# Kernel optimization log

Measured on AMD Instinct MI355X. Metric: run time of the kernel, lower is better.

Reference implementation:

```python
import jax, jax.numpy as jnp
import numpy as np

MAX_SPAN_WIDTH = 12
THRESHOLD = 0.5


def _span_table(num_words):
    starts, ends = [], []
    for s in range(num_words):
        for e in range(s, min(num_words, s + MAX_SPAN_WIDTH)):
            starts.append(s)
            ends.append(e)
    return np.asarray(starts, np.int32), np.asarray(ends, np.int32)


def _mlp(x, w1, b1, w2, b2):
    # Linear -> LeakyReLU(0.01) -> Linear
    return jax.nn.leaky_relu(x @ w1 + b1, negative_slope=0.01) @ w2 + b2


def setup_inputs() -> dict:
    B, L, H, E, W, DFF = 8, 1024, 768, 16, 504, 512
    key = jax.random.key(0)
    ks = jax.random.split(key, 9)
    hidden_states = jax.random.normal(ks[0], (B, L, H), dtype=jnp.float32)
    # layout: first E tokens are entity-type tokens, next 2*W tokens are text (2 subwords/word)
    ent_mask = np.zeros((B, L), np.int32); ent_mask[:, :E] = 1
    text_mask = np.zeros((B, L), np.int32); text_mask[:, E:E + 2 * W] = 1
    word_index = np.full((B, L), -1, np.int32)
    word_index[:, E:E + 2 * W] = np.repeat(np.arange(W, dtype=np.int32), 2)[None, :]
    s = 0.02
    return {
        "hidden_states": hidden_states,
        "ent_w1": jax.random.normal(ks[1], (H, DFF), jnp.float32) * s,
        "ent_b1": jnp.zeros((DFF,), jnp.float32),
        "ent_w2": jax.random.normal(ks[2], (DFF, H), jnp.float32) * s,
        "ent_b2": jnp.zeros((H,), jnp.float32),
        "span_w1": jax.random.normal(ks[3], (2 * H, DFF), jnp.float32) * s,
        "span_b1": jnp.zeros((DFF,), jnp.float32),
        "span_w2": jax.random.normal(ks[4], (DFF, H), jnp.float32) * s,
        "span_b2": jnp.zeros((H,), jnp.float32),
        "text_mask": jnp.asarray(text_mask),
        "ent_mask": jnp.asarray(ent_mask),
        "word_index": jnp.asarray(word_index),
        "num_words": W,
        "num_ent": E,
    }


def reference(hidden_states, ent_w1, ent_b1, ent_w2, ent_b2,
              span_w1, span_b1, span_w2, span_b2,
              text_mask, ent_mask, word_index, num_words, num_ent):
    B, L, H = hidden_states.shape
    W, E = int(num_words), int(num_ent)

    # ---- word-level mean pooling over subword tokens (WordTokenRepresentation) ----
    valid = (text_mask == 1) & (word_index >= 0)                       # [B,L]
    oh = ((word_index[..., None] == jnp.arange(W)) & valid[..., None]).astype(hidden_states.dtype)  # [B,L,W]
    counts = jnp.maximum(oh.sum(axis=1), 1.0)                          # [B,W]
    word_emb = jnp.einsum('blw,blh->bwh', oh, hidden_states) / counts[..., None]

    # ---- gather entity-type tokens in order (EntityTokenRepresentation) ----
    keyv = jnp.where(ent_mask == 1, jnp.arange(L), L + jnp.arange(L))
    ent_pos = jnp.argsort(keyv, axis=-1)[:, :E]                        # [B,E]
    ent_tok = jnp.take_along_axis(hidden_states, ent_pos[..., None], axis=1)  # [B,E,H]
    ent_vec = _mlp(ent_tok, ent_w1, ent_b1, ent_w2, ent_b2)            # [B,E,H]

    # ---- span representations (all spans of width < MAX_SPAN_WIDTH) ----
    starts_np, ends_np = _span_table(W)                                # [N]
    span_in = jnp.concatenate([word_emb[:, starts_np], word_emb[:, ends_np]], axis=-1)  # [B,N,2H]
    span_vec = _mlp(span_in, span_w1, span_b1, span_w2, span_b2)       # [B,N,H]

    # ---- matching logits ----
    logits = jnp.einsum('bnh,beh->bne', span_vec, ent_vec)             # [B,N,E]

    # ---- NMS-style greedy decode (flat mode): threshold + score sort + overlap rejection ----
    N = logits.shape[1]
    probs = jax.nn.sigmoid(logits).reshape(B, N * E)
    cstart = jnp.repeat(jnp.asarray(starts_np), E)                     # [N*E]
    cend = jnp.repeat(jnp.asarray(ends_np), E)
    order = jnp.argsort(-probs, axis=-1)                               # score-descending
    probs_s = jnp.take_along_axis(probs, order, axis=-1)
    s_s, e_s = cstart[order], cend[order]
    pos = jnp.arange(W)

    def decode_one(pr, ss, ee):
        def body(cov, x):
            p, s, e = x
            m = (pos >= s) & (pos <= e)                                # candidate span mask over words
            take = (p > THRESHOLD) & ~jnp.any(cov & m)                 # flat: reject any overlap
            return cov | (m & take), take
        _, taken = jax.lax.scan(body, jnp.zeros((W,), bool), (pr, ss, ee))
        return taken

    taken_sorted = jax.vmap(decode_one)(probs_s, s_s, e_s)             # [B,N*E]
    inv = jnp.argsort(order, axis=-1)
    selected = jnp.take_along_axis(taken_sorted, inv, axis=-1).reshape(B, N, E)
    return logits, selected
```

## Files before the change

### kernel.cpp

```cpp
#include <hip/hip_runtime.h>
#include <hip/hip_bf16.h>
#include <stdint.h>

#define B_ 8
#define L_ 1024
#define H_ 768
#define E_ 16
#define W_ 504
#define DFF_ 512
#define N_ 5982
#define NE_ (N_*E_)
#define BNE_ (B_*NE_)
#define MAXC_ 6144
#define MAXK48 0x0000FFFFFFFFFFFFull
#define PT_ 24

typedef unsigned long long u64;
typedef unsigned int u32;

__device__ __forceinline__ int rowstart_of(int s){
    int s0 = W_ - 11;
    if (s <= s0) return 12*s;
    int t = s - s0;
    return 12*s0 + t*11 - (t*(t-1))/2;
}

__device__ __forceinline__ u64 shflup_u64(u64 x, int d){
    u32 lo = (u32)__shfl_up((int)(u32)x, d, 64);
    u32 hi = (u32)__shfl_up((int)(u32)(x >> 32), d, 64);
    return ((u64)hi << 32) | (u64)lo;
}
__device__ __forceinline__ u64 shflxor_u64(u64 x, int m){
    u32 lo = (u32)__shfl_xor((int)(u32)x, m, 64);
    u32 hi = (u32)__shfl_xor((int)(u32)(x >> 32), m, 64);
    return ((u64)hi << 32) | (u64)lo;
}

__global__ void k_prolog(const int* __restrict__ ent_mask, int* __restrict__ ent_pos,
                         int* __restrict__ starts, int* __restrict__ ends,
                         int* __restrict__ tokc){
    int blk = blockIdx.x; int tid = threadIdx.x;
    if (blk == 8){
        for (int s = tid; s < W_; s += 256){
            int rs = rowstart_of(s);
            int cnt = min(12, W_ - s);
            for (int i = 0; i < cnt; i++){ starts[rs+i] = s; ends[rs+i] = s+i; }
        }
        for (int i = tid; i < B_*W_; i += 256) tokc[i] = 0;
        return;
    }
    __shared__ u32 wt[4]; __shared__ u32 cbase;
    int b = blk;
    int lane = tid & 63, wave = tid >> 6;
    if (tid == 0) cbase = 0;
    __syncthreads();
    for (int base = 0; base < L_; base += 256){
        int l = base + tid;
        bool f = (ent_mask[b*L_ + l] == 1);
        u64 bal = __ballot(f);
        if (lane == 0) wt[wave] = (u32)__popcll(bal);
        __syncthreads();
        u32 pre = cbase;
        for (int w = 0; w < 4; w++) if (w < wave) pre += wt[w];
        if (f){
            u32 rank = pre + (u32)__popcll(bal & ((1ull<<lane)-1ull));
            if (rank < E_) ent_pos[b*E_ + rank] = l;
        }
        __syncthreads();
        if (tid == 0){ u32 r = cbase; for (int w = 0; w < 4; w++) r += wt[w]; cbase = r; }
        __syncthreads();
    }
    u32 totEnt = cbase;
    if (totEnt >= E_) return;
    for (int base = 0; base < L_; base += 256){
        int l = base + tid;
        bool f = (ent_mask[b*L_ + l] != 1);
        u64 bal = __ballot(f);
        if (lane == 0) wt[wave] = (u32)__popcll(bal);
        __syncthreads();
        u32 pre = cbase;
        for (int w = 0; w < 4; w++) if (w < wave) pre += wt[w];
        if (f){
            u32 rank = pre + (u32)__popcll(bal & ((1ull<<lane)-1ull));
            if (rank < E_) ent_pos[b*E_ + rank] = l;
        }
        __syncthreads();
        if (tid == 0){ u32 r = cbase; for (int w = 0; w < 4; w++) r += wt[w]; cbase = r; }
        __syncthreads();
    }
}

__global__ void k_toklist(const int* __restrict__ tm, const int* __restrict__ wi,
                          int* __restrict__ tok, int* __restrict__ tokc){
    int i = blockIdx.x*256 + threadIdx.x;
    if (i >= B_*L_) return;
    int w = wi[i];
    if (tm[i] == 1 && w >= 0 && w < W_){
        int b = i / L_;
        int bw = b*W_ + w;
        int pos = atomicAdd(&tokc[bw], 1);
        if (pos < 4) tok[bw*4 + pos] = i - b*L_;
    }
}

__global__ void k_poolsort(const float* __restrict__ hs, const int* __restrict__ tok,
                           const int* __restrict__ tokc, float* __restrict__ wemb){
    __shared__ int stok[4]; __shared__ int scnt;
    int bw = blockIdx.x;
    int b = bw / W_;
    int tid = threadIdx.x;
    if (tid == 0){
        int c = tokc[bw]; int cc = min(c, 4);
        int v[4];
        for (int k = 0; k < cc; k++) v[k] = tok[bw*4 + k];
        for (int a = 1; a < cc; a++){ int x = v[a]; int j = a-1; while (j >= 0 && v[j] > x){ v[j+1] = v[j]; j--; } v[j+1] = x; }
        for (int k = 0; k < cc; k++) stok[k] = v[k];
        scnt = c;
    }
    __syncthreads();
    int c = scnt; int cc = min(c, 4);
    float denom = (float)max(c, 1);
    for (int h = tid; h < H_; h += 256){
        double s = 0.0;
        for (int k = 0; k < cc; k++)
            s += (double)hs[((size_t)(b*L_ + stok[k]))*H_ + h];
        wemb[(size_t)bw*H_ + h] = (float)(s / (double)denom);
    }
}

__global__ void k_ent1(const float* __restrict__ hs, const int* __restrict__ ent_pos,
                       const float* __restrict__ w1, const float* __restrict__ b1,
                       float* __restrict__ hidg){
    __shared__ float x[H_];
    int blk = blockIdx.x;
    int be = blk >> 1; int half = blk & 1;
    int b = be >> 4;
    int tid = threadIdx.x;
    int pos = ent_pos[be];
    const float* xp = hs + ((size_t)b*L_ + pos)*H_;
    for (int j = tid; j < H_; j += 256) x[j] = xp[j];
    __syncthreads();
    int d = half*256 + tid;
    float a0=0.f,a1=0.f,a2=0.f,a3=0.f;
    const float* wp = w1 + d;
    #pragma unroll 8
    for (int h = 0; h < H_; h += 4){
        a0 += x[h+0]*wp[(size_t)(h+0)*DFF_];
        a1 += x[h+1]*wp[(size_t)(h+1)*DFF_];
        a2 += x[h+2]*wp[(size_t)(h+2)*DFF_];
        a3 += x[h+3]*wp[(size_t)(h+3)*DFF_];
    }
    float acc = ((a0+a1)+(a2+a3)) + b1[d];
    hidg[(size_t)be*DFF_ + d] = acc > 0.f ? acc : 0.01f*acc;
}

__global__ void k_ent2(const float* __restrict__ hidg,
                       const float* __restrict__ w2, const float* __restrict__ b2,
                       float* __restrict__ ent_vec){
    __shared__ float hsd[DFF_];
    int blk = blockIdx.x;
    int be = blk / 3; int third = blk % 3;
    int tid = threadIdx.x;
    const float* hp = hidg + (size_t)be*DFF_;
    for (int j = tid; j < DFF_; j += 256) hsd[j] = hp[j];
    __syncthreads();
    int j = third*256 + tid;
    float a0=0.f,a1=0.f,a2=0.f,a3=0.f;
    const float* wp = w2 + j;
    #pragma unroll 8
    for (int d = 0; d < DFF_; d += 4){
        a0 += hsd[d+0]*wp[(size_t)(d+0)*H_];
        a1 += hsd[d+1]*wp[(size_t)(d+1)*H_];
        a2 += hsd[d+2]*wp[(size_t)(d+2)*H_];
        a3 += hsd[d+3]*wp[(size_t)(d+3)*H_];
    }
    ent_vec[(size_t)be*H_ + j] = ((a0+a1)+(a2+a3)) + b2[j];
}

__global__ void k_Mc(const float* __restrict__ span_w2, const float* __restrict__ span_b2,
                     const float* __restrict__ ent_vec, float* __restrict__ M,
                     float* __restrict__ cvec){
    int blk = blockIdx.x;
    if (blk == 256){
        int i = threadIdx.x;
        if (i < B_*E_){
            const float* ev = ent_vec + (size_t)i*H_;
            double acc = 0.0;
            for (int h = 0; h < H_; h++) acc += (double)span_b2[h]*(double)ev[h];
            cvec[i] = (float)acc;
        }
        return;
    }
    int b = blk/32; int dbase = (blk%32)*16;
    int tid = threadIdx.x; int d = dbase + (tid>>4); int e = tid&15;
    const float* ev = ent_vec + ((size_t)b*E_ + e)*H_;
    const float* wr = span_w2 + (size_t)d*H_;
    double p0=0.0, p1=0.0;
    for (int h = 0; h < H_; h += 2){
        p0 += (double)wr[h]*(double)ev[h];
        p1 += (double)wr[h+1]*(double)ev[h+1];
    }
    M[((size_t)b*DFF_ + d)*E_ + e] = (float)(p0+p1);
}

__global__ void k_pq(const float* __restrict__ wemb, const float* __restrict__ w1,
                     float* __restrict__ PQ, int b0){
    __shared__ float As[16][68];
    __shared__ float Bs[16][68];
    int bx = blockIdx.x & 15;
    int by = blockIdx.x >> 4;
    int tid = threadIdx.x;
    int tm = tid >> 4, tn = tid & 15;
    const float* A0 = wemb + (size_t)b0*W_*H_;
    int colbase = bx*64;
    const float* Bbase = (colbase < DFF_) ? w1 : (w1 + (size_t)H_*DFF_);
    int bcol0 = (colbase < DFF_) ? colbase : (colbase - DFF_);
    float acc[4][4] = {{0.f}};
    int ar = tid >> 2, akq = tid & 3;
    int bkk = tid >> 4, bcq = tid & 15;
    const int ROWS = 4*W_;
    for (int k0 = 0; k0 < H_; k0 += 16){
        {
            int gr = by*64 + ar;
            float4 av;
            if (gr < ROWS) av = *(const float4*)(A0 + (size_t)gr*H_ + k0 + akq*4);
            else av = make_float4(0.f,0.f,0.f,0.f);
            As[akq*4+0][ar] = av.x; As[akq*4+1][ar] = av.y;
            As[akq*4+2][ar] = av.z; As[akq*4+3][ar] = av.w;
        }
        {
            float4 bv = *(const float4*)(Bbase + (size_t)(k0+bkk)*DFF_ + bcol0 + bcq*4);
            Bs[bkk][bcq*4+0] = bv.x; Bs[bkk][bcq*4+1] = bv.y;
            Bs[bkk][bcq*4+2] = bv.z; Bs[bkk][bcq*4+3] = bv.w;
        }
        __syncthreads();
        #pragma unroll
        for (int kk = 0; kk < 16; kk++){
            float4 a = *(const float4*)&As[kk][tm*4];
            float4 bv = *(const float4*)&Bs[kk][tn*4];
            acc[0][0] += a.x*bv.x; acc[0][1] += a.x*bv.y; acc[0][2] += a.x*bv.z; acc[0][3] += a.x*bv.w;
            acc[1][0] += a.y*bv.x; acc[1][1] += a.y*bv.y; acc[1][2] += a.y*bv.z; acc[1][3] += a.y*bv.w;
            acc[2][0] += a.z*bv.x; acc[2][1] += a.z*bv.y; acc[2][2] += a.z*bv.z; acc[2][3] += a.z*bv.w;
            acc[3][0] += a.w*bv.x; acc[3][1] += a.w*bv.y; acc[3][2] += a.w*bv.z; acc[3][3] += a.w*bv.w;
        }
        __syncthreads();
    }
    #pragma unroll
    for (int r = 0; r < 4; r++){
        int gr = by*64 + tm*4 + r;
        if (gr < ROWS){
            float4 ov = make_float4(acc[r][0], acc[r][1], acc[r][2], acc[r][3]);
            *(float4*)(PQ + (size_t)gr*1024 + colbase + tn*4) = ov;
        }
    }
}

__global__ void k_logits(const float* __restrict__ PQ, const float* __restrict__ Mmat,
                         const float* __restrict__ cvec, const float* __restrict__ span_b1,
                         float* __restrict__ logits, float* __restrict__ outL, int b0){
    __shared__ float Ps[DFF_];
    __shared__ float hid[DFF_];
    __shared__ double redw[64];
    __shared__ float csh[E_];
    int blk = blockIdx.x;
    int bl = blk / W_; int s = blk - bl*W_;
    int b = b0 + bl;
    int tid = threadIdx.x;
    int lane = tid & 63, wave = tid >> 6;
    int ee = tid & 15; int g = tid >> 4;
    float Mreg[32];
    {
        const float* Mp = Mmat + (size_t)b*DFF_*E_ + (size_t)(g*32)*E_ + ee;
        #pragma unroll
        for (int i = 0; i < 32; i++) Mreg[i] = Mp[(size_t)i*E_];
    }
    const float* P = PQ + ((size_t)(bl*W_ + s))*1024;
    for (int d = tid; d < DFF_; d += 256) Ps[d] = P[d] + span_b1[d];
    if (tid < E_) csh[tid] = cvec[b*E_ + tid];
    __syncthreads();
    int nsp = min(12, W_ - s);
    int nbase = rowstart_of(s);
    for (int i = 0; i < nsp; i++){
        int e = s + i;
        const float* Q = PQ + ((size_t)(bl*W_ + e))*1024 + DFF_;
        for (int d = tid; d < DFF_; d += 256){
            float h = Ps[d] + Q[d];
            hid[d] = h > 0.f ? h : 0.01f*h;
        }
        __syncthreads();
        {
            int d0 = g*32;
            double a0=0.0, a1=0.0, a2=0.0, a3=0.0;
            #pragma unroll
            for (int k = 0; k < 32; k += 4){
                a0 += (double)hid[d0+k+0]*(double)Mreg[k+0];
                a1 += (double)hid[d0+k+1]*(double)Mreg[k+1];
                a2 += (double)hid[d0+k+2]*(double)Mreg[k+2];
                a3 += (double)hid[d0+k+3]*(double)Mreg[k+3];
            }
            double acc = (a0+a1)+(a2+a3);
            double t = acc + __shfl_down(acc, 32, 64);
            t = t + __shfl_down(t, 16, 64);
            if (lane < 16) redw[wave*16 + lane] = t;
        }
        __syncthreads();
        if (tid < E_){
            double t = ((redw[tid] + redw[16+tid]) + (redw[32+tid] + redw[48+tid]))
                     + (double)csh[tid];
            float lg = (float)t;
            size_t oi = ((size_t)b*N_ + nbase + i)*E_ + tid;
            logits[oi] = lg;
            outL[oi] = lg;
        }
        __syncthreads();
    }
}

__global__ void k_spanbest(const float* __restrict__ logits,
                           const int* __restrict__ starts, const int* __restrict__ ends,
                           u64* __restrict__ candS, float* __restrict__ outSel){
    int idx = blockIdx.x*256 + threadIdx.x;
    if (idx >= B_*N_) return;
    int b = idx / N_; int n = idx - b*N_;
    const float* lg = logits + (size_t)b*NE_ + (size_t)n*16;
    u64 best = ~0ull;
    for (int e = 0; e < 16; e++){
        float prob = 1.0f/(1.0f + expf(-lg[e]));
        if (prob > 0.5f){
            u32 key24 = (~__float_as_uint(prob)) & 0xFFFFFFu;
            u64 pk = ((u64)key24 << 24) | (u64)(u32)(n*16 + e);
            best = best < pk ? best : pk;
        }
    }
    int s = starts[n], e2 = ends[n];
    int len = e2 - s + 1;
    u64 packed = best;
    if (best != ~0ull)
        packed = best | ((u64)(u32)s << 48) | ((u64)(u32)(len-1) << 57);
    candS[idx] = packed;
    float* selp = outSel + (size_t)BNE_ + (size_t)b*NE_ + (size_t)n*16;
    float4 z = make_float4(0.f,0.f,0.f,0.f);
    *(float4*)(selp+0)  = z; *(float4*)(selp+4)  = z;
    *(float4*)(selp+8)  = z; *(float4*)(selp+12) = z;
}

__device__ __forceinline__ void decode_wave(const u64* sp, int n,
                                            float* __restrict__ outSel, int b){
    int lane = threadIdx.x & 63;
    u64 scov[8];
    #pragma unroll
    for (int k = 0; k < 8; k++) scov[k] = 0ull;
    int covcnt = 0;
    for (int base = 0; base < n; base += 64){
        int i = base + lane;
        bool has = i < n;
        u64 v = has ? sp[i] : ~0ull;
        int s   = (int)((v >> 48) & 0x1FFull);
        int len = (int)((v >> 57) & 0xFull) + 1;
        u32 c   = (u32)(v & 0xFFFFFFull);
        int w0 = s >> 6, sh0 = s & 63;
        int w1i = (w0 < 7) ? w0 + 1 : 7;
        u64 full = (1ull << len) - 1ull;
        u64 m0 = has ? (full << sh0) : 0ull;
        u64 m1 = (has && sh0 + len > 64) ? (full >> (64 - sh0)) : 0ull;
        u64 myc0 = 0ull, myc1 = 0ull;
        #pragma unroll
        for (int k = 0; k < 8; k++){
            if (w0  == k) myc0 = scov[k];
            if (w1i == k) myc1 = scov[k];
        }
        bool alive = has && (((myc0 & m0) | (myc1 & m1)) == 0ull);
        bool accept = false;
        u64 balv = __ballot(alive);
        if (balv){
            u64 pm[8];
            #pragma unroll
            for (int k = 0; k < 8; k++){
                u64 t = 0ull;
                if (alive){
                    if (w0  == k) t |= m0;
                    if (w1i == k) t |= m1;
                }
                pm[k] = t;
            }
            #pragma unroll
            for (int st = 1; st < 64; st <<= 1){
                #pragma unroll
                for (int k = 0; k < 8; k++) pm[k] |= shflup_u64(pm[k], st);
            }
            u64 ex0 = 0ull, ex1 = 0ull;
            #pragma unroll
            for (int k = 0; k < 8; k++){
                u64 e = shflup_u64(pm[k], 1);
                e = (lane == 0) ? 0ull : e;
                if (w0  == k) ex0 = e;
                if (w1i == k) ex1 = e;
            }
            bool blocked = (((ex0 & m0) | (ex1 & m1)) != 0ull);
            bool newacc = alive && !blocked;
            accept = newacc;
            u64 am[8];
            #pragma unroll
            for (int k = 0; k < 8; k++){
                u64 t = 0ull;
                if (newacc){
                    if (w0  == k) t |= m0;
                    if (w1i == k) t |= m1;
                }
                am[k] = t;
            }
            #pragma unroll
            for (int st = 1; st < 64; st <<= 1){
                #pragma unroll
                for (int k = 0; k < 8; k++) am[k] |= shflxor_u64(am[k], st);
            }
            #pragma unroll
            for (int k = 0; k < 8; k++){
                covcnt += (int)__popcll(am[k]);
                scov[k] |= am[k];
            }
            u64 pend = __ballot(alive && blocked);
            u32 vlo = (u32)v, vhi = (u32)(v >> 32);
            u64 accm = 0ull;
            while (pend){
                int j = (int)__builtin_ctzll(pend);
                pend &= pend - 1ull;
#if __has_builtin(__builtin_amdgcn_readlane)
                u32 jlo = (u32)__builtin_amdgcn_readlane((int)vlo, j);
                u32 jhi = (u32)__builtin_amdgcn_readlane((int)vhi, j);
#else
                u32 jlo = (u32)__shfl((int)vlo, j, 64);
                u32 jhi = (u32)__shfl((int)vhi, j, 64);
#endif
                u64 jv = ((u64)jhi << 32) | (u64)jlo;
                int js   = (int)((jv >> 48) & 0x1FFull);
                int jlen = (int)((jv >> 57) & 0xFull) + 1;
                int jw0 = js >> 6, jsh = js & 63;
                int jw1 = (jw0 < 7) ? jw0 + 1 : 7;
                u64 jfull = (1ull << jlen) - 1ull;
                u64 jm0 = jfull << jsh;
                u64 jm1 = (jsh + jlen > 64) ? (jfull >> (64 - jsh)) : 0ull;
                u64 c0 = 0ull, c1 = 0ull;
                #pragma unroll
                for (int k = 0; k < 8; k++){
                    if (jw0 == k) c0 = scov[k];
                    if (jw1 == k) c1 = scov[k];
                }
                bool ok = (((c0 & jm0) | (c1 & jm1)) == 0ull);
                u64 okm = ok ? ~0ull : 0ull;
                #pragma unroll
                for (int k = 0; k < 8; k++){
                    u64 add = 0ull;
                    if (jw0 == k) add |= jm0;
                    if (jw1 == k) add |= jm1;
                    scov[k] |= (add & okm);
                }
                covcnt += ok ? jlen : 0;
                accm |= (okm & (1ull << j));
            }
            if (((accm >> lane) & 1ull) != 0ull) accept = true;
        }
        if (accept)
            outSel[(size_t)BNE_ + (size_t)b*NE_ + (size_t)c] = 1.0f;
        if (covcnt >= W_) break;
    }
}

__global__ __launch_bounds__(256) void k_tailA(const u64* __restrict__ candS,
                                               u64* __restrict__ candO, int* __restrict__ cntp){
    __shared__ u64 cs[6032];
    __shared__ u64 Ma[512], Mb[512];
    __shared__ u32 wtot[4];
    __shared__ int nsh;
    int b = blockIdx.x; int tid = threadIdx.x;
    int lane = tid & 63, wave = tid >> 6;
    const u64* cSg = candS + (size_t)b*N_;

    #pragma unroll
    for (int k = 0; k < 23; k++) cs[tid + k*256] = cSg[tid + k*256];
    { int i23 = tid + 23*256; if (i23 < N_) cs[i23] = cSg[i23]; }
    __syncthreads();

    for (int s = tid; s < 512; s += 256)
        Ma[s] = (s < W_) ? (cs[rowstart_of(s)] & MAXK48) : MAXK48;
    __syncthreads();
    u64* Mcur = Ma; u64* Mnext = Mb;
    for (int l = 2; l <= 12; l++){
        #pragma unroll
        for (int q = 0; q < 2; q++){
            int s = tid + q*256;
            u64 key = MAXK48; int idx = -1;
            if (s + l <= W_){ idx = rowstart_of(s) + (l-1); key = cs[idx] & MAXK48; }
            u64 a = Mcur[s];
            u64 bb = (s + 1 < 512) ? Mcur[s+1] : MAXK48;
            u64 dom = a < bb ? a : bb;
            if (idx >= 0 && dom < key) cs[idx] = ~0ull;
            Mnext[s] = dom < key ? dom : key;
        }
        __syncthreads();
        u64* t = Mcur; Mcur = Mnext; Mnext = t;
    }

    {
        int base = tid*PT_;
        u64 vv[PT_];
        u32 flags = 0; int cnt = 0;
        #pragma unroll
        for (int k = 0; k < PT_; k++){
            int i = base + k;
            u64 v = (i < N_) ? cs[i] : ~0ull;
            vv[k] = v;
            if (v != ~0ull){ flags |= (1u << k); cnt++; }
        }
        u32 inc = (u32)cnt;
        for (int d = 1; d < 64; d <<= 1){ u32 o = (u32)__shfl_up((int)inc, d, 64); if (lane >= d) inc += o; }
        if (lane == 63) wtot[wave] = inc;
        __syncthreads();
        u32 woffs = 0;
        for (int w = 0; w < 4; w++) if (w < wave) woffs += wtot[w];
        u32 off = woffs + inc - (u32)cnt;
        if (tid == 255) nsh = (int)(woffs + inc);
        #pragma unroll
        for (int k = 0; k < PT_; k++){
            if (flags & (1u << k)) cs[off++] = vv[k];
        }
    }
    __syncthreads();
    int n = nsh;
    if (tid < 16) cs[n + tid] = ~0ull;
    __syncthreads();

    if (n <= 1536){
        u64 v0=~0ull,v1=~0ull,v2=~0ull,v3=~0ull,v4=~0ull,v5=~0ull;
        u64 k0=0,k1=0,k2=0,k3=0,k4=0,k5=0;
        if (tid        < n){ v0 = cs[tid];        k0 = v0 & MAXK48; }
        if (tid +  256 < n){ v1 = cs[tid +  256]; k1 = v1 & MAXK48; }
        if (tid +  512 < n){ v2 = cs[tid +  512]; k2 = v2 & MAXK48; }
        if (tid +  768 < n){ v3 = cs[tid +  768]; k3 = v3 & MAXK48; }
        if (tid + 1024 < n){ v4 = cs[tid + 1024]; k4 = v4 & MAXK48; }
        if (tid + 1280 < n){ v5 = cs[tid + 1280]; k5 = v5 & MAXK48; }
        u32 r0=0,r1=0,r2=0,r3=0,r4=0,r5=0;
        for (int j = 0; j < n; j += 16){
            u64 c0 = cs[j+ 0]&MAXK48, c1 = cs[j+ 1]&MAXK48, c2 = cs[j+ 2]&MAXK48, c3 = cs[j+ 3]&MAXK48;
            u64 c4 = cs[j+ 4]&MAXK48, c5 = cs[j+ 5]&MAXK48, c6 = cs[j+ 6]&MAXK48, c7 = cs[j+ 7]&MAXK48;
            u64 c8 = cs[j+ 8]&MAXK48, c9 = cs[j+ 9]&MAXK48, cA = cs[j+10]&MAXK48, cB = cs[j+11]&MAXK48;
            u64 cC = cs[j+12]&MAXK48, cD = cs[j+13]&MAXK48, cE = cs[j+14]&MAXK48, cF = cs[j+15]&MAXK48;
            r0 += (u32)(c0<k0)+(u32)(c1<k0)+(u32)(c2<k0)+(u32)(c3<k0)+(u32)(c4<k0)+(u32)(c5<k0)+(u32)(c6<k0)+(u32)(c7<k0)
                + (u32)(c8<k0)+(u32)(c9<k0)+(u32)(cA<k0)+(u32)(cB<k0)+(u32)(cC<k0)+(u32)(cD<k0)+(u32)(cE<k0)+(u32)(cF<k0);
            r1 += (u32)(c0<k1)+(u32)(c1<k1)+(u32)(c2<k1)+(u32)(c3<k1)+(u32)(c4<k1)+(u32)(c5<k1)+(u32)(c6<k1)+(u32)(c7<k1)
                + (u32)(c8<k1)+(u32)(c9<k1)+(u32)(cA<k1)+(u32)(cB<k1)+(u32)(cC<k1)+(u32)(cD<k1)+(u32)(cE<k1)+(u32)(cF<k1);
            r2 += (u32)(c0<k2)+(u32)(c1<k2)+(u32)(c2<k2)+(u32)(c3<k2)+(u32)(c4<k2)+(u32)(c5<k2)+(u32)(c6<k2)+(u32)(c7<k2)
                + (u32)(c8<k2)+(u32)(c9<k2)+(u32)(cA<k2)+(u32)(cB<k2)+(u32)(cC<k2)+(u32)(cD<k2)+(u32)(cE<k2)+(u32)(cF<k2);
            r3 += (u32)(c0<k3)+(u32)(c1<k3)+(u32)(c2<k3)+(u32)(c3<k3)+(u32)(c4<k3)+(u32)(c5<k3)+(u32)(c6<k3)+(u32)(c7<k3)
                + (u32)(c8<k3)+(u32)(c9<k3)+(u32)(cA<k3)+(u32)(cB<k3)+(u32)(cC<k3)+(u32)(cD<k3)+(u32)(cE<k3)+(u32)(cF<k3);
            r4 += (u32)(c0<k4)+(u32)(c1<k4)+(u32)(c2<k4)+(u32)(c3<k4)+(u32)(c4<k4)+(u32)(c5<k4)+(u32)(c6<k4)+(u32)(c7<k4)
                + (u32)(c8<k4)+(u32)(c9<k4)+(u32)(cA<k4)+(u32)(cB<k4)+(u32)(cC<k4)+(u32)(cD<k4)+(u32)(cE<k4)+(u32)(cF<k4);
            r5 += (u32)(c0<k5)+(u32)(c1<k5)+(u32)(c2<k5)+(u32)(c3<k5)+(u32)(c4<k5)+(u32)(c5<k5)+(u32)(c6<k5)+(u32)(c7<k5)
                + (u32)(c8<k5)+(u32)(c9<k5)+(u32)(cA<k5)+(u32)(cB<k5)+(u32)(cC<k5)+(u32)(cD<k5)+(u32)(cE<k5)+(u32)(cF<k5);
        }
        __syncthreads();
        if (tid        < n) cs[r0] = v0;
        if (tid +  256 < n) cs[r1] = v1;
        if (tid +  512 < n) cs[r2] = v2;
        if (tid +  768 < n) cs[r3] = v3;
        if (tid + 1024 < n) cs[r4] = v4;
        if (tid + 1280 < n) cs[r5] = v5;
        __syncthreads();
    } else {
        u64 vv[PT_]; u32 rr[PT_];
        #pragma unroll
        for (int k = 0; k < PT_; k++){ vv[k] = ~0ull; rr[k] = 0; }
        #pragma unroll
        for (int k = 0; k < PT_; k++){
            int i = tid + (k << 8);
            if (i < n){
                u64 v = cs[i];
                vv[k] = v;
                u64 ki = v & MAXK48;
                u32 r = 0;
                for (int j = 0; j < n; j += 8){
                    u64 c0 = cs[j+0]&MAXK48, c1 = cs[j+1]&MAXK48;
                    u64 c2 = cs[j+2]&MAXK48, c3 = cs[j+3]&MAXK48;
                    u64 c4 = cs[j+4]&MAXK48, c5 = cs[j+5]&MAXK48;
                    u64 c6 = cs[j+6]&MAXK48, c7 = cs[j+7]&MAXK48;
                    r += (u32)(c0<ki) + (u32)(c1<ki) + (u32)(c2<ki) + (u32)(c3<ki)
                       + (u32)(c4<ki) + (u32)(c5<ki) + (u32)(c6<ki) + (u32)(c7<ki);
                }
                rr[k] = r;
            }
        }
        __syncthreads();
        #pragma unroll
        for (int k = 0; k < PT_; k++){
            int i = tid + (k << 8);
            if (i < n) cs[rr[k]] = vv[k];
        }
        __syncthreads();
    }

    for (int i = tid; i < n; i += 256) candO[(size_t)b*MAXC_ + i] = cs[i];
    if (tid == 0) cntp[b] = n;
}

__global__ __launch_bounds__(64) void k_tailB(const u64* __restrict__ candO,
                                              const int* __restrict__ cntp,
                                              float* __restrict__ outSel){
    __shared__ u64 cs[MAXC_];
    int b = blockIdx.x; int lane = threadIdx.x;
    int n = cntp[b];
    const u64* src = candO + (size_t)b*MAXC_;
    for (int i = lane; i < n; i += 64) cs[i] = src[i];
    __syncthreads();
    decode_wave(cs, n, outSel, b);
}

extern "C" void kernel_launch(void* const* d_in, const int* in_sizes, int n_in,
                              void* d_out, int out_size, void* d_ws, size_t ws_size,
                              hipStream_t stream){
    const float* hs        = (const float*)d_in[0];
    const float* ent_w1    = (const float*)d_in[1];
    const float* ent_b1    = (const float*)d_in[2];
    const float* ent_w2    = (const float*)d_in[3];
    const float* ent_b2    = (const float*)d_in[4];
    const float* span_w1   = (const float*)d_in[5];
    const float* span_b1   = (const float*)d_in[6];
    const float* span_w2   = (const float*)d_in[7];
    const float* span_b2   = (const float*)d_in[8];
    const int*  text_mask  = (const int*)d_in[9];
    const int*  ent_mask   = (const int*)d_in[10];
    const int*  word_index = (const int*)d_in[11];
    float* out = (float*)d_out;

    char* wsbase = (char*)d_ws; size_t off = 0;
    auto alloc = [&](size_t bytes)->void*{ void* p = wsbase + off; off = (off + bytes + 255) & ~(size_t)255; return p; };
    char*  region1 = (char*)alloc((size_t)B_*W_*H_*4);
    float* wemb   = (float*)region1;
    u64*   candS  = (u64*)region1;
    u64*   candO  = (u64*)(region1 + 393216);
    int*   tok    = (int*)  alloc((size_t)B_*W_*4*4);
    int*   tokc   = (int*)  alloc((size_t)B_*W_*4);
    float* PQ     = (float*)alloc((size_t)4*W_*1024*4);
    float* logits = (float*)alloc((size_t)BNE_*4);
    int*   entpos = (int*)  alloc((size_t)B_*E_*4);
    float* hidg   = (float*)alloc((size_t)B_*E_*DFF_*4);
    float* entvec = (float*)alloc((size_t)B_*E_*H_*4);
    float* Mmat   = (float*)alloc((size_t)B_*DFF_*E_*4);
    float* cvec   = (float*)alloc((size_t)B_*E_*4);
    int*   starts = (int*)  alloc((size_t)N_*4);
    int*   ends   = (int*)  alloc((size_t)N_*4);
    int*   cntp   = (int*)  alloc((size_t)B_*4);

    k_prolog<<<9,256,0,stream>>>(ent_mask, entpos, starts, ends, tokc);
    k_toklist<<<(B_*L_+255)/256,256,0,stream>>>(text_mask, word_index, tok, tokc);
    k_poolsort<<<B_*W_,256,0,stream>>>(hs, tok, tokc, wemb);
    k_ent1<<<B_*E_*2,256,0,stream>>>(hs, entpos, ent_w1, ent_b1, hidg);
    k_ent2<<<B_*E_*3,256,0,stream>>>(hidg, ent_w2, ent_b2, entvec);
    k_Mc<<<257,256,0,stream>>>(span_w2, span_b2, entvec, Mmat, cvec);
    for (int b0 = 0; b0 < B_; b0 += 4){
        k_pq<<<512,256,0,stream>>>(wemb, span_w1, PQ, b0);
        k_logits<<<4*W_,256,0,stream>>>(PQ, Mmat, cvec, span_b1, logits, out, b0);
    }
    k_spanbest<<<(B_*N_+255)/256,256,0,stream>>>(logits, starts, ends, candS, out);
    k_tailA<<<B_,256,0,stream>>>(candS, candO, cntp);
    k_tailB<<<B_,64,0,stream>>>(candO, cntp, out);
}
```

Baseline: 443.3 us.

## Double-buffer k_pq GEMM loads and add local-max pruning round to NMS decode

The k_pq GEMM tile depth grows from 16 to 32, and the next tile's global loads are prefetched into registers while the current tile is being computed, which hides load latency and halves the number of barriers. The NMS decode kernel gains an extra pruning pass. It computes a per-word minimum key over covering candidates, marks words claimed by candidates that are local minima, and kills every candidate dominated by a claimed word. This shrinks the candidate list before the compaction and serial greedy stage. It costs more shared-memory work per block plus extra barriers, and the pruning is only correct if the dominance reasoning holds.

```diff
diff --git a/kernel.cpp b/kernel.cpp
--- a/kernel.cpp
+++ b/kernel.cpp
@@ -205,8 +205,8 @@
 
 __global__ void k_pq(const float* __restrict__ wemb, const float* __restrict__ w1,
                      float* __restrict__ PQ, int b0){
-    __shared__ float As[16][68];
-    __shared__ float Bs[16][68];
+    __shared__ float As[32][68];
+    __shared__ float Bs[32][68];
     int bx = blockIdx.x & 15;
     int by = blockIdx.x >> 4;
     int tid = threadIdx.x;
@@ -219,23 +219,34 @@
     int ar = tid >> 2, akq = tid & 3;
     int bkk = tid >> 4, bcq = tid & 15;
     const int ROWS = 4*W_;
-    for (int k0 = 0; k0 < H_; k0 += 16){
-        {
-            int gr = by*64 + ar;
-            float4 av;
-            if (gr < ROWS) av = *(const float4*)(A0 + (size_t)gr*H_ + k0 + akq*4);
-            else av = make_float4(0.f,0.f,0.f,0.f);
-            As[akq*4+0][ar] = av.x; As[akq*4+1][ar] = av.y;
-            As[akq*4+2][ar] = av.z; As[akq*4+3][ar] = av.w;
-        }
-        {
-            float4 bv = *(const float4*)(Bbase + (size_t)(k0+bkk)*DFF_ + bcol0 + bcq*4);
-            Bs[bkk][bcq*4+0] = bv.x; Bs[bkk][bcq*4+1] = bv.y;
-            Bs[bkk][bcq*4+2] = bv.z; Bs[bkk][bcq*4+3] = bv.w;
-        }
-        __syncthreads();
-        #pragma unroll
-        for (int kk = 0; kk < 16; kk++){
+    int gr = by*64 + ar;
+    bool aok = (gr < ROWS);
+    const float* Ap = A0 + (size_t)gr*H_ + akq*4;
+    const float* Bp = Bbase + (size_t)bkk*DFF_ + bcol0 + bcq*4;
+    float4 av0, av1, bv0, bv1;
+    av0 = aok ? *(const float4*)(Ap + 0)  : make_float4(0.f,0.f,0.f,0.f);
+    av1 = aok ? *(const float4*)(Ap + 16) : make_float4(0.f,0.f,0.f,0.f);
+    bv0 = *(const float4*)(Bp + 0);
+    bv1 = *(const float4*)(Bp + (size_t)16*DFF_);
+    for (int k0 = 0; k0 < H_; k0 += 32){
+        As[akq*4+0][ar] = av0.x; As[akq*4+1][ar] = av0.y;
+        As[akq*4+2][ar] = av0.z; As[akq*4+3][ar] = av0.w;
+        As[16+akq*4+0][ar] = av1.x; As[16+akq*4+1][ar] = av1.y;
+        As[16+akq*4+2][ar] = av1.z; As[16+akq*4+3][ar] = av1.w;
+        Bs[bkk][bcq*4+0] = bv0.x; Bs[bkk][bcq*4+1] = bv0.y;
+        Bs[bkk][bcq*4+2] = bv0.z; Bs[bkk][bcq*4+3] = bv0.w;
+        Bs[16+bkk][bcq*4+0] = bv1.x; Bs[16+bkk][bcq*4+1] = bv1.y;
+        Bs[16+bkk][bcq*4+2] = bv1.z; Bs[16+bkk][bcq*4+3] = bv1.w;
+        __syncthreads();
+        if (k0 + 32 < H_){
+            int kn = k0 + 32;
+            av0 = aok ? *(const float4*)(Ap + kn)      : make_float4(0.f,0.f,0.f,0.f);
+            av1 = aok ? *(const float4*)(Ap + kn + 16) : make_float4(0.f,0.f,0.f,0.f);
+            bv0 = *(const float4*)(Bp + (size_t)kn*DFF_);
+            bv1 = *(const float4*)(Bp + (size_t)(kn+16)*DFF_);
+        }
+        #pragma unroll
+        for (int kk = 0; kk < 32; kk++){
             float4 a = *(const float4*)&As[kk][tm*4];
             float4 bv = *(const float4*)&Bs[kk][tn*4];
             acc[0][0] += a.x*bv.x; acc[0][1] += a.x*bv.y; acc[0][2] += a.x*bv.z; acc[0][3] += a.x*bv.w;
@@ -247,10 +258,10 @@
     }
     #pragma unroll
     for (int r = 0; r < 4; r++){
-        int gr = by*64 + tm*4 + r;
-        if (gr < ROWS){
+        int grr = by*64 + tm*4 + r;
+        if (grr < ROWS){
             float4 ov = make_float4(acc[r][0], acc[r][1], acc[r][2], acc[r][3]);
-            *(float4*)(PQ + (size_t)gr*1024 + colbase + tn*4) = ov;
+            *(float4*)(PQ + (size_t)grr*1024 + colbase + tn*4) = ov;
         }
     }
 }
@@ -500,6 +511,59 @@
         __syncthreads();
         u64* t = Mcur; Mcur = Mnext; Mnext = t;
     }
+    __syncthreads();
+
+    {
+        for (int w = tid; w < 512; w += 256){
+            u64 m = ~0ull;
+            if (w < W_){
+                int slo = (w > 11) ? (w - 11) : 0;
+                for (int s = slo; s <= w; s++){
+                    int rs = rowstart_of(s);
+                    int lmax = min(12, W_ - s);
+                    for (int l = w - s + 1; l <= lmax; l++){
+                        u64 kk2 = cs[rs + l - 1] & MAXK48;
+                        if (kk2 < m) m = kk2;
+                    }
+                }
+            }
+            Ma[w] = m;
+        }
+        for (int w = tid; w < 512; w += 256) Mb[w] = ~0ull;
+        __syncthreads();
+        for (int k = 0; k < PT_; k++){
+            int i = tid + (k << 8);
+            if (i < N_){
+                u64 v = cs[i];
+                if (v != ~0ull){
+                    int s = (int)((v >> 48) & 0x1FFull);
+                    int len = (int)((v >> 57) & 0xFull) + 1;
+                    u64 key = v & MAXK48;
+                    u64 rmin = ~0ull;
+                    for (int w = s; w < s + len; w++){ u64 t = Ma[w]; if (t < rmin) rmin = t; }
+                    if (rmin == key){
+                        for (int w = s; w < s + len; w++) Mb[w] = key;
+                    }
+                }
+            }
+        }
+        __syncthreads();
+        for (int k = 0; k < PT_; k++){
+            int i = tid + (k << 8);
+            if (i < N_){
+                u64 v = cs[i];
+                if (v != ~0ull){
+                    int s = (int)((v >> 48) & 0x1FFull);
+                    int len = (int)((v >> 57) & 0xFull) + 1;
+                    u64 key = v & MAXK48;
+                    bool kill = false;
+                    for (int w = s; w < s + len; w++) kill = kill || (Mb[w] < key);
+                    if (kill) cs[i] = ~0ull;
+                }
+            }
+        }
+        __syncthreads();
+    }
 
     {
         int base = tid*PT_;
```

After: 429.2 us. 3.2% less time.
